# Kernel tuning notes

Measured on AMD Instinct MI355X. Metric: run time of the kernel, lower is better.

Reference implementation:

```python
import jax, jax.numpy as jnp
import numpy as np

H = 1024      # hidden_size
I = 2 * H     # intermediate_size (expand_factor=2)
N = 16        # ssm_state_size
K = 4         # conv_kernel
BATCH = 2
SEQ = 2048


def setup_inputs() -> dict:
    key = jax.random.key(0)
    k = jax.random.split(key, 6)
    x = jax.random.normal(k[0], (BATCH, SEQ, H), dtype=jnp.float32)
    # nn.Linear default init ~ U(-1/sqrt(fan_in), 1/sqrt(fan_in)); scale is fine for a reference
    W_in = jax.random.normal(k[1], (2 * I, H), dtype=jnp.float32) / np.sqrt(H)
    conv_w = jax.random.normal(k[2], (I, 1, K), dtype=jnp.float32) / np.sqrt(K)
    W_x = jax.random.normal(k[3], (2 * N + 1, I), dtype=jnp.float32) / np.sqrt(I)
    A_log = jax.random.normal(k[4], (I, N), dtype=jnp.float32)
    D = jnp.ones((I,), dtype=jnp.float32)
    W_out = jax.random.normal(k[5], (H, I), dtype=jnp.float32) / np.sqrt(I)
    return {"x": x, "W_in": W_in, "conv_w": conv_w, "W_x": W_x,
            "A_log": A_log, "D": D, "W_out": W_out}


def reference(x, W_in, conv_w, W_x, A_log, D, W_out):
    xz = jnp.einsum('bsh,ih->bsi', x, W_in)
    xp, z = jnp.split(xz, 2, axis=-1)
    # depthwise causal conv1d: pad left K-1 (torch pads both sides then slices [:S])
    xc = jax.lax.conv_general_dilated(
        xp.transpose(0, 2, 1),           # (B, I, S)
        conv_w,                          # (I, 1, K) = OIH with groups=I
        window_strides=(1,),
        padding=[(K - 1, 0)],
        feature_group_count=I,
        dimension_numbers=('NCH', 'OIH', 'NCH'),
    ).transpose(0, 2, 1)                 # (B, S, I)
    xc = jax.nn.silu(xc)
    # x_proj -> delta (1), B (N), C (N)
    xproj = jnp.einsum('bsi,pi->bsp', xc, W_x)   # (B,S,2N+1)
    delta = jax.nn.softplus(xproj[..., :1])       # (B,S,1)
    Bmat = xproj[..., 1:1 + N]                    # (B,S,N)
    Cmat = xproj[..., 1 + N:]                     # (B,S,N)
    A = -jnp.exp(A_log)                           # (I,N)
    # decay/states broadcast-reduce: (B,S,I,N) intermediates reduced over N
    decay = jnp.exp(delta[..., None] * A[None, None])            # (B,S,I,N)
    states = xc[..., None] * Bmat[:, :, None, :] * decay          # (B,S,I,N)
    y = jnp.sum(states * Cmat[:, :, None, :], axis=-1)            # (B,S,I)
    y = y + xc * D[None, None, :]
    return jnp.einsum('bsi,hi->bsh', y * jax.nn.silu(z), W_out)
```

## Files before the change

### kernel.cpp

```cpp
#include <hip/hip_runtime.h>

#define LOG2E 1.4426950408889634f

__device__ __forceinline__ float b2f(unsigned short u) {
    unsigned int v = ((unsigned int)u) << 16;
    return __builtin_bit_cast(float, v);
}
__device__ __forceinline__ unsigned short f2b(float f) {
    unsigned int u = __builtin_bit_cast(unsigned int, f);
    u += 0x7fffu + ((u >> 16) & 1u);
    return (unsigned short)(u >> 16);
}
__device__ __forceinline__ float fexp(float x) {
    return __builtin_amdgcn_exp2f(x * LOG2E);
}
__device__ __forceinline__ float silu_f(float x) {
    return x * __builtin_amdgcn_rcpf(1.0f + fexp(-x));
}
__device__ __forceinline__ unsigned short u4get(ushort4 v, int c) {
    return c == 0 ? v.x : c == 1 ? v.y : c == 2 ? v.z : v.w;
}

typedef const __attribute__((address_space(1))) unsigned int* gas_t;
typedef __attribute__((address_space(3))) unsigned int* las_t;
__device__ __forceinline__ void gl2lds16(const unsigned short* g, unsigned short* l) {
    __builtin_amdgcn_global_load_lds((gas_t)(const void*)g, (las_t)(void*)l, 16, 0, 0);
}

typedef __bf16 bf16x8 __attribute__((ext_vector_type(8)));
typedef float  fx4    __attribute__((ext_vector_type(4)));
typedef int    ix4    __attribute__((ext_vector_type(4)));
union FragU { ix4 i; bf16x8 b; };

__global__ __launch_bounds__(256) void cast_xw_k(const float* __restrict__ x,
                                                 const float* __restrict__ W_in,
                                                 unsigned short* __restrict__ xb,
                                                 unsigned short* __restrict__ wib) {
    int b = blockIdx.x;
    const float* src = (b < 4096) ? x : W_in;
    unsigned short* dst = (b < 4096) ? xb : wib;
    int i = (b & 4095) * 256 + threadIdx.x;
    float4 v = ((const float4*)src)[i];
    *(ushort4*)(dst + (size_t)i * 4) = make_ushort4(f2b(v.x), f2b(v.y), f2b(v.z), f2b(v.w));
}

__global__ __launch_bounds__(256) void gemm1_cast_k(const unsigned short* __restrict__ A,
                                                    const unsigned short* __restrict__ B,
                                                    unsigned short* __restrict__ C,
                                                    const float* __restrict__ W_out,
                                                    const float* __restrict__ W_x,
                                                    const float* __restrict__ Alog,
                                                    unsigned short* __restrict__ wob,
                                                    unsigned short* __restrict__ wxb,
                                                    float* __restrict__ A2) {
    const int bid = blockIdx.x;
    if (bid < 2146) {
        if (bid < 2048) {
            int i = bid * 256 + threadIdx.x;
            float4 v = ((const float4*)W_out)[i];
            *(ushort4*)(wob + (size_t)i * 4) = make_ushort4(f2b(v.x), f2b(v.y), f2b(v.z), f2b(v.w));
        } else if (bid < 2114) {
            int i = (bid - 2048) * 256 + threadIdx.x;
            float4 v = ((const float4*)W_x)[i];
            *(ushort4*)(wxb + (size_t)i * 4) = make_ushort4(f2b(v.x), f2b(v.y), f2b(v.z), f2b(v.w));
        } else {
            int i = (bid - 2114) * 256 + threadIdx.x;
            float4 v = ((const float4*)Alog)[i];
            ((float4*)A2)[i] = make_float4(-fexp(v.x) * LOG2E, -fexp(v.y) * LOG2E,
                                           -fexp(v.z) * LOG2E, -fexp(v.w) * LOG2E);
        }
        return;
    }
    const int g = bid - 2146;
    const int N = 4096, K = 1024;
    __shared__ __align__(16) unsigned short sA[128 * 64];
    __shared__ __align__(16) unsigned short sB[128 * 64];
    const int tid  = threadIdx.x;
    const int lane = tid & 63, wave = tid >> 6;
    const int bm = (g >> 5) * 128, bn = (g & 31) * 128;
    const int wm = (wave >> 1) * 64, wn = (wave & 1) * 64;
    const int row16 = lane & 15, quad = lane >> 4;
    const int srow = lane >> 3;
    const int sc16 = (lane & 7) ^ srow;
    const unsigned short* gA = A + (size_t)(bm + wave * 32 + srow) * K + sc16 * 8;
    const unsigned short* gB = B + (size_t)(bn + wave * 32 + srow) * K + sc16 * 8;
    unsigned short* lA = sA + (wave * 4) * 512;
    unsigned short* lB = sB + (wave * 4) * 512;
    fx4 acc[4][4] = {};

    for (int kt = 0; kt < K; kt += 64) {
#pragma unroll
        for (int it = 0; it < 4; ++it) {
            gl2lds16(gA + (size_t)it * 8 * K + kt, lA + it * 512);
            gl2lds16(gB + (size_t)it * 8 * K + kt, lB + it * 512);
        }
        __syncthreads();
#pragma unroll
        for (int kk = 0; kk < 64; kk += 32) {
            FragU af[4], bf[4];
#pragma unroll
            for (int t = 0; t < 4; ++t) {
                int ra = wm + t * 16 + row16;
                af[t].i = *(const ix4*)(sA + ra * 64 + ((quad + (kk >> 3)) ^ (ra & 7)) * 8);
            }
#pragma unroll
            for (int t = 0; t < 4; ++t) {
                int rb = wn + t * 16 + row16;
                bf[t].i = *(const ix4*)(sB + rb * 64 + ((quad + (kk >> 3)) ^ (rb & 7)) * 8);
            }
#pragma unroll
            for (int tm = 0; tm < 4; ++tm)
#pragma unroll
                for (int tn = 0; tn < 4; ++tn)
                    acc[tm][tn] = __builtin_amdgcn_mfma_f32_16x16x32_bf16(
                        af[tm].b, bf[tn].b, acc[tm][tn], 0, 0, 0);
        }
        __syncthreads();
    }
#pragma unroll
    for (int tm = 0; tm < 4; ++tm) {
        int row0 = bm + wm + tm * 16 + quad * 4;
#pragma unroll
        for (int tn = 0; tn < 4; ++tn) {
            int col = bn + wn + tn * 16 + row16;
#pragma unroll
            for (int r = 0; r < 4; ++r)
                C[(size_t)(row0 + r) * N + col] = f2b(acc[tm][tn][r]);
        }
    }
}

__global__ __launch_bounds__(256) void gemm_bt_64(const unsigned short* __restrict__ A,
                                                  const unsigned short* __restrict__ B,
                                                  float* __restrict__ C, int N, int K) {
    __shared__ __align__(16) unsigned short sA[64 * 64];
    __shared__ __align__(16) unsigned short sB[64 * 64];
    const int tid  = threadIdx.x;
    const int lane = tid & 63, wave = tid >> 6;
    const int bm = blockIdx.y * 64, bn = blockIdx.x * 64;
    const int wm = wave * 16;
    const int row16 = lane & 15, quad = lane >> 4;
    const int srow = lane >> 3;
    const int sc16 = (lane & 7) ^ srow;
    const unsigned short* gA = A + (size_t)(bm + wave * 16 + srow) * K + sc16 * 8;
    const unsigned short* gB = B + (size_t)(bn + wave * 16 + srow) * K + sc16 * 8;
    unsigned short* lA = sA + (wave * 2) * 512;
    unsigned short* lB = sB + (wave * 2) * 512;
    fx4 acc[4] = {};

    for (int kt = 0; kt < K; kt += 64) {
#pragma unroll
        for (int it = 0; it < 2; ++it) {
            gl2lds16(gA + (size_t)it * 8 * K + kt, lA + it * 512);
            gl2lds16(gB + (size_t)it * 8 * K + kt, lB + it * 512);
        }
        __syncthreads();
#pragma unroll
        for (int kk = 0; kk < 64; kk += 32) {
            FragU af, bf[4];
            int ra = wm + row16;
            af.i = *(const ix4*)(sA + ra * 64 + ((quad + (kk >> 3)) ^ (ra & 7)) * 8);
#pragma unroll
            for (int t = 0; t < 4; ++t) {
                int rb = t * 16 + row16;
                bf[t].i = *(const ix4*)(sB + rb * 64 + ((quad + (kk >> 3)) ^ (rb & 7)) * 8);
            }
#pragma unroll
            for (int tn = 0; tn < 4; ++tn)
                acc[tn] = __builtin_amdgcn_mfma_f32_16x16x32_bf16(af.b, bf[tn].b, acc[tn], 0, 0, 0);
        }
        __syncthreads();
    }
    const int row0 = bm + wm + quad * 4;
#pragma unroll
    for (int tn = 0; tn < 4; ++tn) {
        int col = bn + tn * 16 + row16;
#pragma unroll
        for (int r = 0; r < 4; ++r)
            C[(size_t)(row0 + r) * N + col] = acc[tn][r];
    }
}

__global__ __launch_bounds__(256) void conv_xproj_k(const unsigned short* __restrict__ xz,
                                                    const float* __restrict__ cw,
                                                    const unsigned short* __restrict__ wxb,
                                                    float* __restrict__ dg) {
    __shared__ __align__(16) unsigned short sxc[8 * 2048];
    __shared__ float sX[4][16][49];
    const int tid  = threadIdx.x;
    const int lane = tid & 63, wave = tid >> 6;
    const int row16 = lane & 15, quad = lane >> 4;
    const int m0 = blockIdx.x * 8, s0 = m0 & 2047;

    {
        ushort4 ua[11], ub[11];
#pragma unroll
        for (int t = 0; t < 11; ++t) {
            int mr = (s0 - 3 + t >= 0) ? (m0 - 3 + t) : m0;
            const unsigned short* p = xz + (size_t)mr * 4096 + tid * 8;
            ua[t] = *(const ushort4*)p;
            ub[t] = *(const ushort4*)(p + 4);
        }
        float w[8][4];
        const float4* cw4 = (const float4*)cw;
#pragma unroll
        for (int c = 0; c < 8; ++c) {
            float4 t4 = cw4[tid * 8 + c];
            w[c][0] = t4.x; w[c][1] = t4.y; w[c][2] = t4.z; w[c][3] = t4.w;
        }
#pragma unroll
        for (int t = 0; t < 3; ++t)
            if (s0 - 3 + t < 0) { ua[t] = make_ushort4(0, 0, 0, 0); ub[t] = make_ushort4(0, 0, 0, 0); }
#pragma unroll
        for (int j = 0; j < 8; ++j) {
            float acc[8] = {0, 0, 0, 0, 0, 0, 0, 0};
#pragma unroll
            for (int k = 0; k < 4; ++k) {
                ushort4 a = ua[j + k], b = ub[j + k];
                float v[8] = {b2f(a.x), b2f(a.y), b2f(a.z), b2f(a.w),
                              b2f(b.x), b2f(b.y), b2f(b.z), b2f(b.w)};
#pragma unroll
                for (int c = 0; c < 8; ++c) acc[c] += v[c] * w[c][k];
            }
            unsigned short* q = sxc + j * 2048 + ((tid ^ (j & 7)) * 8);
            *(ushort4*)q       = make_ushort4(f2b(silu_f(acc[0])), f2b(silu_f(acc[1])),
                                              f2b(silu_f(acc[2])), f2b(silu_f(acc[3])));
            *(ushort4*)(q + 4) = make_ushort4(f2b(silu_f(acc[4])), f2b(silu_f(acc[5])),
                                              f2b(silu_f(acc[6])), f2b(silu_f(acc[7])));
        }
    }
    __syncthreads();

    {
        fx4 acc[3] = {};
        const unsigned short* bp = wxb + (size_t)row16 * 2048 + wave * 512 + quad * 8;
        const int arow = row16 & 7;
        const int cbase = wave * 64 + quad;
#pragma unroll 4
        for (int kk = 0; kk < 512; kk += 32) {
            FragU a, b0, b1, b2;
            int c16 = cbase + (kk >> 3);
            a.i  = *(const ix4*)(sxc + arow * 2048 + ((c16 ^ arow) * 8));
            b0.i = *(const ix4*)(bp + kk);
            b1.i = *(const ix4*)(bp + 16 * 2048 + kk);
            b2.i = *(const ix4*)(bp + 32 * 2048 + kk);
            acc[0] = __builtin_amdgcn_mfma_f32_16x16x32_bf16(a.b, b0.b, acc[0], 0, 0, 0);
            acc[1] = __builtin_amdgcn_mfma_f32_16x16x32_bf16(a.b, b1.b, acc[1], 0, 0, 0);
            acc[2] = __builtin_amdgcn_mfma_f32_16x16x32_bf16(a.b, b2.b, acc[2], 0, 0, 0);
        }
#pragma unroll
        for (int t = 0; t < 3; ++t)
#pragma unroll
            for (int r = 0; r < 4; ++r)
                sX[wave][quad * 4 + r][t * 16 + row16] = acc[t][r];
    }
    __syncthreads();
    for (int idx = tid; idx < 136; idx += 256) {
        int rr = idx / 17, q = idx - rr * 17;
        float o;
        if (q == 0) {
            float v = sX[0][rr][0] + sX[1][rr][0] + sX[2][rr][0] + sX[3][rr][0];
            o = (v > 20.f) ? v : log1pf(fexp(v));
        } else {
            float bs = sX[0][rr][q]      + sX[1][rr][q]      + sX[2][rr][q]      + sX[3][rr][q];
            float cs = sX[0][rr][q + 16] + sX[1][rr][q + 16] + sX[2][rr][q + 16] + sX[3][rr][q + 16];
            o = bs * cs;
        }
        dg[(size_t)(m0 + rr) * 17 + q] = o;
    }
}

__global__ __launch_bounds__(256, 2) void conv_ssm_k(const unsigned short* __restrict__ xz,
                                                     const float* __restrict__ cw,
                                                     const float* __restrict__ dg,
                                                     const float* __restrict__ A2,
                                                     const float* __restrict__ Dv,
                                                     unsigned short* __restrict__ y2) {
    __shared__ float sdg[4 * 17];
    const int tid = threadIdx.x;
    const int m0 = blockIdx.y * 4, s0 = m0 & 2047;
    const int ch0 = blockIdx.x * 1024 + tid * 4;
    if (tid < 68) sdg[tid] = dg[(size_t)m0 * 17 + tid];

    ushort4 uw[7];
#pragma unroll
    for (int t = 0; t < 7; ++t) {
        int mr = (s0 - 3 + t >= 0) ? (m0 - 3 + t) : m0;
        uw[t] = *(const ushort4*)(xz + (size_t)mr * 4096 + ch0);
    }
    ushort4 zu[4];
#pragma unroll
    for (int j = 0; j < 4; ++j)
        zu[j] = *(const ushort4*)(xz + (size_t)(m0 + j) * 4096 + 2048 + ch0);
    float w[4][4];
    const float4* cw4 = (const float4*)cw;
#pragma unroll
    for (int c = 0; c < 4; ++c) {
        float4 t4 = cw4[ch0 + c];
        w[c][0] = t4.x; w[c][1] = t4.y; w[c][2] = t4.z; w[c][3] = t4.w;
    }
    float a2[4][16];
#pragma unroll
    for (int c = 0; c < 4; ++c) {
        const float4* ar = (const float4*)(A2 + (size_t)(ch0 + c) * 16);
#pragma unroll
        for (int n4 = 0; n4 < 4; ++n4) {
            float4 t4 = ar[n4];
            a2[c][n4 * 4 + 0] = t4.x; a2[c][n4 * 4 + 1] = t4.y;
            a2[c][n4 * 4 + 2] = t4.z; a2[c][n4 * 4 + 3] = t4.w;
        }
    }
    float4 dvv = *(const float4*)(Dv + ch0);
    float dv[4] = {dvv.x, dvv.y, dvv.z, dvv.w};
#pragma unroll
    for (int t = 0; t < 3; ++t)
        if (s0 - 3 + t < 0) uw[t] = make_ushort4(0, 0, 0, 0);
    __syncthreads();

#pragma unroll
    for (int j = 0; j < 4; ++j) {
        float delta = sdg[j * 17];
        float Gr[16];
#pragma unroll
        for (int n = 0; n < 16; ++n) Gr[n] = sdg[j * 17 + 1 + n];
        unsigned short ov[4];
#pragma unroll
        for (int c = 0; c < 4; ++c) {
            float acc = 0.f;
#pragma unroll
            for (int k = 0; k < 4; ++k)
                acc += b2f(u4get(uw[j + k], c)) * w[c][k];
            float xc = silu_f(acc);
            float ssum = 0.f;
#pragma unroll
            for (int n = 0; n < 16; ++n)
                ssum += Gr[n] * __builtin_amdgcn_exp2f(delta * a2[c][n]);
            float y = xc * (dv[c] + ssum);
            ov[c] = f2b(y * silu_f(b2f(u4get(zu[j], c))));
        }
        *(ushort4*)(y2 + (size_t)(m0 + j) * 2048 + ch0) = make_ushort4(ov[0], ov[1], ov[2], ov[3]);
    }
}

extern "C" void kernel_launch(void* const* d_in, const int* in_sizes, int n_in,
                              void* d_out, int out_size, void* d_ws, size_t ws_size,
                              hipStream_t stream) {
    const float* x      = (const float*)d_in[0];
    const float* W_in   = (const float*)d_in[1];
    const float* conv_w = (const float*)d_in[2];
    const float* W_x    = (const float*)d_in[3];
    const float* A_log  = (const float*)d_in[4];
    const float* Dvec   = (const float*)d_in[5];
    const float* W_out  = (const float*)d_in[6];

    char* ws = (char*)d_ws;
    unsigned short* xb  = (unsigned short*)(ws);
    unsigned short* wib = (unsigned short*)(ws + 8388608);
    unsigned short* wob = (unsigned short*)(ws + 16777216);
    unsigned short* xz  = (unsigned short*)(ws + 20971520);
    unsigned short* y2  = (unsigned short*)(ws + 54525952);
    unsigned short* wxb = (unsigned short*)(ws + 71303168);
    float*          dgp = (float*)        (ws + 71499776);
    float*          a2p = (float*)        (ws + 71778304);

    cast_xw_k<<<8192, 256, 0, stream>>>(x, W_in, xb, wib);
    gemm1_cast_k<<<3170, 256, 0, stream>>>(xb, wib, xz, W_out, W_x, A_log, wob, wxb, a2p);
    conv_xproj_k<<<512, 256, 0, stream>>>(xz, conv_w, wxb, dgp);
    conv_ssm_k<<<dim3(2, 1024), 256, 0, stream>>>(xz, conv_w, dgp, a2p, Dvec, y2);
    gemm_bt_64<<<dim3(16, 64), 256, 0, stream>>>(y2, wob, (float*)d_out, 1024, 2048);
}
```

Before: 208.7 us.

## Store conv+silu output once and reuse it in the SSM gate kernel

The xproj kernel now writes its bf16 conv+silu result to a global workspace buffer, and the SSM kernel reads that buffer instead of recomputing the depthwise conv from the raw xz rows. The conv_xproj kernel also handles 4 rows per block instead of 8 and launches twice as many blocks. This removes the duplicated conv work and the 7-row halo loads in the SSM kernel, at the cost of an extra 8 MB global write and read. The smaller tile raises block count, but halo overhead per output row grows in the conv stage.

```diff
diff --git a/kernel.cpp b/kernel.cpp
--- a/kernel.cpp
+++ b/kernel.cpp
@@ -184,18 +184,19 @@
 __global__ __launch_bounds__(256) void conv_xproj_k(const unsigned short* __restrict__ xz,
                                                     const float* __restrict__ cw,
                                                     const unsigned short* __restrict__ wxb,
+                                                    unsigned short* __restrict__ xcb,
                                                     float* __restrict__ dg) {
-    __shared__ __align__(16) unsigned short sxc[8 * 2048];
+    __shared__ __align__(16) unsigned short sxc[4 * 2048];
     __shared__ float sX[4][16][49];
     const int tid  = threadIdx.x;
     const int lane = tid & 63, wave = tid >> 6;
     const int row16 = lane & 15, quad = lane >> 4;
-    const int m0 = blockIdx.x * 8, s0 = m0 & 2047;
+    const int m0 = blockIdx.x * 4, s0 = m0 & 2047;
 
     {
-        ushort4 ua[11], ub[11];
-#pragma unroll
-        for (int t = 0; t < 11; ++t) {
+        ushort4 ua[7], ub[7];
+#pragma unroll
+        for (int t = 0; t < 7; ++t) {
             int mr = (s0 - 3 + t >= 0) ? (m0 - 3 + t) : m0;
             const unsigned short* p = xz + (size_t)mr * 4096 + tid * 8;
             ua[t] = *(const ushort4*)p;
@@ -212,7 +213,7 @@
         for (int t = 0; t < 3; ++t)
             if (s0 - 3 + t < 0) { ua[t] = make_ushort4(0, 0, 0, 0); ub[t] = make_ushort4(0, 0, 0, 0); }
 #pragma unroll
-        for (int j = 0; j < 8; ++j) {
+        for (int j = 0; j < 4; ++j) {
             float acc[8] = {0, 0, 0, 0, 0, 0, 0, 0};
 #pragma unroll
             for (int k = 0; k < 4; ++k) {
@@ -222,11 +223,16 @@
 #pragma unroll
                 for (int c = 0; c < 8; ++c) acc[c] += v[c] * w[c][k];
             }
-            unsigned short* q = sxc + j * 2048 + ((tid ^ (j & 7)) * 8);
-            *(ushort4*)q       = make_ushort4(f2b(silu_f(acc[0])), f2b(silu_f(acc[1])),
-                                              f2b(silu_f(acc[2])), f2b(silu_f(acc[3])));
-            *(ushort4*)(q + 4) = make_ushort4(f2b(silu_f(acc[4])), f2b(silu_f(acc[5])),
-                                              f2b(silu_f(acc[6])), f2b(silu_f(acc[7])));
+            ushort4 o0 = make_ushort4(f2b(silu_f(acc[0])), f2b(silu_f(acc[1])),
+                                      f2b(silu_f(acc[2])), f2b(silu_f(acc[3])));
+            ushort4 o1 = make_ushort4(f2b(silu_f(acc[4])), f2b(silu_f(acc[5])),
+                                      f2b(silu_f(acc[6])), f2b(silu_f(acc[7])));
+            unsigned short* q = sxc + j * 2048 + ((tid ^ (j & 3)) * 8);
+            *(ushort4*)q       = o0;
+            *(ushort4*)(q + 4) = o1;
+            unsigned short* g = xcb + (size_t)(m0 + j) * 2048 + tid * 8;
+            *(ushort4*)g       = o0;
+            *(ushort4*)(g + 4) = o1;
         }
     }
     __syncthreads();
@@ -234,7 +240,7 @@
     {
         fx4 acc[3] = {};
         const unsigned short* bp = wxb + (size_t)row16 * 2048 + wave * 512 + quad * 8;
-        const int arow = row16 & 7;
+        const int arow = row16 & 3;
         const int cbase = wave * 64 + quad;
 #pragma unroll 4
         for (int kk = 0; kk < 512; kk += 32) {
@@ -255,7 +261,7 @@
                 sX[wave][quad * 4 + r][t * 16 + row16] = acc[t][r];
     }
     __syncthreads();
-    for (int idx = tid; idx < 136; idx += 256) {
+    for (int idx = tid; idx < 68; idx += 256) {
         int rr = idx / 17, q = idx - rr * 17;
         float o;
         if (q == 0) {
@@ -270,34 +276,23 @@
     }
 }
 
-__global__ __launch_bounds__(256, 2) void conv_ssm_k(const unsigned short* __restrict__ xz,
-                                                     const float* __restrict__ cw,
+__global__ __launch_bounds__(256, 2) void ssm_gate_k(const unsigned short* __restrict__ xz,
+                                                     const unsigned short* __restrict__ xcb,
                                                      const float* __restrict__ dg,
                                                      const float* __restrict__ A2,
                                                      const float* __restrict__ Dv,
                                                      unsigned short* __restrict__ y2) {
     __shared__ float sdg[4 * 17];
     const int tid = threadIdx.x;
-    const int m0 = blockIdx.y * 4, s0 = m0 & 2047;
+    const int m0 = blockIdx.y * 4;
     const int ch0 = blockIdx.x * 1024 + tid * 4;
     if (tid < 68) sdg[tid] = dg[(size_t)m0 * 17 + tid];
 
-    ushort4 uw[7];
-#pragma unroll
-    for (int t = 0; t < 7; ++t) {
-        int mr = (s0 - 3 + t >= 0) ? (m0 - 3 + t) : m0;
-        uw[t] = *(const ushort4*)(xz + (size_t)mr * 4096 + ch0);
-    }
-    ushort4 zu[4];
-#pragma unroll
-    for (int j = 0; j < 4; ++j)
+    ushort4 xu[4], zu[4];
+#pragma unroll
+    for (int j = 0; j < 4; ++j) {
+        xu[j] = *(const ushort4*)(xcb + (size_t)(m0 + j) * 2048 + ch0);
         zu[j] = *(const ushort4*)(xz + (size_t)(m0 + j) * 4096 + 2048 + ch0);
-    float w[4][4];
-    const float4* cw4 = (const float4*)cw;
-#pragma unroll
-    for (int c = 0; c < 4; ++c) {
-        float4 t4 = cw4[ch0 + c];
-        w[c][0] = t4.x; w[c][1] = t4.y; w[c][2] = t4.z; w[c][3] = t4.w;
     }
     float a2[4][16];
 #pragma unroll
@@ -312,9 +307,6 @@
     }
     float4 dvv = *(const float4*)(Dv + ch0);
     float dv[4] = {dvv.x, dvv.y, dvv.z, dvv.w};
-#pragma unroll
-    for (int t = 0; t < 3; ++t)
-        if (s0 - 3 + t < 0) uw[t] = make_ushort4(0, 0, 0, 0);
     __syncthreads();
 
 #pragma unroll
@@ -326,11 +318,7 @@
         unsigned short ov[4];
 #pragma unroll
         for (int c = 0; c < 4; ++c) {
-            float acc = 0.f;
-#pragma unroll
-            for (int k = 0; k < 4; ++k)
-                acc += b2f(u4get(uw[j + k], c)) * w[c][k];
-            float xc = silu_f(acc);
+            float xc = b2f(u4get(xu[j], c));
             float ssum = 0.f;
 #pragma unroll
             for (int n = 0; n < 16; ++n)
@@ -362,10 +350,11 @@
     unsigned short* wxb = (unsigned short*)(ws + 71303168);
     float*          dgp = (float*)        (ws + 71499776);
     float*          a2p = (float*)        (ws + 71778304);
+    unsigned short* xcb = (unsigned short*)(ws + 71909376);
 
     cast_xw_k<<<8192, 256, 0, stream>>>(x, W_in, xb, wib);
     gemm1_cast_k<<<3170, 256, 0, stream>>>(xb, wib, xz, W_out, W_x, A_log, wob, wxb, a2p);
-    conv_xproj_k<<<512, 256, 0, stream>>>(xz, conv_w, wxb, dgp);
-    conv_ssm_k<<<dim3(2, 1024), 256, 0, stream>>>(xz, conv_w, dgp, a2p, Dvec, y2);
+    conv_xproj_k<<<1024, 256, 0, stream>>>(xz, conv_w, wxb, xcb, dgp);
+    ssm_gate_k<<<dim3(2, 1024), 256, 0, stream>>>(xz, xcb, dgp, a2p, Dvec, y2);
     gemm_bt_64<<<dim3(16, 64), 256, 0, stream>>>(y2, wob, (float*)d_out, 1024, 2048);
 }
```

Measured after the change: 219.1 us. +5.0%, slower.
